# Kernel tuning notes

Measured on AMD Instinct MI355X. Metric: run time of the kernel, lower is better.

Reference implementation:

```python
import jax, jax.numpy as jnp
import numpy as np

N, E = 50000, 500000
DH, DL = 13, 128          # handcrafted / learned node feature dims
OH, OL = 32, 96           # node-encoder output dims; node_dim D = OH+OL
D = OH + OL               # 128
EIN = (DH + DL) + 1 + 3 * D + 1  # 527, forced by concat in forward
H = 256                   # MLP hidden width
HC = 64                   # classifier hidden width
EPS = 1e-8


def _mlp(x, W1, b1, W2, b2):
    # 2-layer MLP with ReLU, matching repo MLP(fc_dims=[H, out])
    return jax.nn.relu(x @ W1 + b1) @ W2 + b2


def _cosine(a, b):
    # torch.nn.CosineSimilarity(dim=1, eps=1e-8)
    na = jnp.maximum(jnp.linalg.norm(a, axis=-1), EPS)
    nb = jnp.maximum(jnp.linalg.norm(b, axis=-1), EPS)
    return jnp.sum(a * b, axis=-1) / (na * nb)


def _lin(key, fan_in, fan_out):
    kW, kb = jax.random.split(key)
    s = 1.0 / np.sqrt(fan_in)
    return (jax.random.uniform(kW, (fan_in, fan_out), jnp.float32, -s, s),
            jax.random.uniform(kb, (fan_out,), jnp.float32, -s, s))


def setup_inputs() -> dict:
    key = jax.random.key(0)
    ks = jax.random.split(key, 16)
    x1 = jax.random.normal(ks[0], (N, DH), jnp.float32)
    x2 = jax.random.normal(ks[1], (N, DL), jnp.float32)
    edge_index = jax.random.randint(ks[2], (2, E), 0, N, jnp.int64)
    Wh1, bh1 = _lin(ks[3], DH, H);   Wh2, bh2 = _lin(ks[4], H, OH)
    Wl1, bl1 = _lin(ks[5], DL, H);   Wl2, bl2 = _lin(ks[6], H, OL)
    We1, be1 = _lin(ks[7], EIN, H);  We2, be2 = _lin(ks[8], H, D)
    Wmsg, bmsg = _lin(ks[9], 2 * D, D)
    Wnode, bnode = _lin(ks[10], 2 * D, D)
    Wmp1, bmp1 = _lin(ks[11], 3 * D, H); Wmp2, bmp2 = _lin(ks[12], H, D)
    Wc1, bc1 = _lin(ks[13], D, HC);  Wc2, bc2 = _lin(ks[14], HC, 1)
    return dict(x1=x1, x2=x2, edge_index=edge_index,
                Wh1=Wh1, bh1=bh1, Wh2=Wh2, bh2=bh2,
                Wl1=Wl1, bl1=bl1, Wl2=Wl2, bl2=bl2,
                We1=We1, be1=be1, We2=We2, be2=be2,
                Wmsg=Wmsg, bmsg=bmsg, Wnode=Wnode, bnode=bnode,
                Wmp1=Wmp1, bmp1=bmp1, Wmp2=Wmp2, bmp2=bmp2,
                Wc1=Wc1, bc1=bc1, Wc2=Wc2, bc2=bc2)


def reference(x1, x2, edge_index,
              Wh1, bh1, Wh2, bh2,
              Wl1, bl1, Wl2, bl2,
              We1, be1, We2, be2,
              Wmsg, bmsg, Wnode, bnode,
              Wmp1, bmp1, Wmp2, bmp2,
              Wc1, bc1, Wc2, bc2):
    src, trg = edge_index[0], edge_index[1]
    # raw-feature edge descriptors
    x_init = jnp.concatenate((x1, x2), axis=-1)            # [N, 141]
    xi_s, xi_t = x_init[src], x_init[trg]                  # gathers [E, 141]
    sim1 = _cosine(xi_s, xi_t)                             # [E]
    abs_init = jnp.abs(xi_s - xi_t)                        # [E, 141]
    # node encoders
    h1 = _mlp(x1, Wh1, bh1, Wh2, bh2)                      # [N, 32]
    h2 = _mlp(x2, Wl1, bl1, Wl2, bl2)                      # [N, 96]
    x = jnp.concatenate((h1, h2), axis=-1)                 # [N, 128]
    xs, xt = x[src], x[trg]                                # [E, 128]
    sim2 = _cosine(xs, xt)                                 # [E]
    edge_feat_in = jnp.concatenate(
        (abs_init, sim1[:, None], xs, xt, jnp.abs(xs - xt), sim2[:, None]),
        axis=-1)                                           # [E, 527]
    e = _mlp(edge_feat_in, We1, be1, We2, be2)             # [E, 128]
    # edge MPNN round: edge->node aggregation, node update, edge update
    msg = jax.nn.relu(jnp.concatenate((xs, e), axis=-1) @ Wmsg + bmsg)  # [E, 128]
    agg = jax.ops.segment_sum(msg, trg, num_segments=N)    # [N, 128]
    xn = jax.nn.relu(jnp.concatenate((x, agg), axis=-1) @ Wnode + bnode)  # [N, 128]
    e_mp = _mlp(jnp.concatenate((xn[src], xn[trg], e), axis=-1),
                Wmp1, bmp1, Wmp2, bmp2)                    # [E, 128]
    pred = _mlp(e_mp, Wc1, bc1, Wc2, bc2)                  # [E, 1]
    return jnp.squeeze(pred, axis=-1)                      # [E]
```

## Files before the change

kernel.cpp:

```cpp
#include <hip/hip_runtime.h>
#include <hip/hip_bf16.h>
#include <hip/hip_fp16.h>


using fp16 = __half;
typedef _Float16 h16;
typedef _Float16 f16x8 __attribute__((ext_vector_type(8)));
typedef _Float16 h16x2 __attribute__((ext_vector_type(2)));
typedef short s16x8 __attribute__((ext_vector_type(8)));
typedef float f32x4 __attribute__((ext_vector_type(4)));

#define NN 50000
#define EE 500000
#define EPSC 1e-8f
#define SCAN_B 196

__device__ __forceinline__ float reluf(float v){ return v > 0.f ? v : 0.f; }

__device__ __forceinline__ float dot8(const f16x8 a, const f16x8 b, float acc)
{
#pragma unroll
  for (int i = 0; i < 4; ++i) {
    const h16x2 av = {a[2 * i], a[2 * i + 1]};
    const h16x2 bv = {b[2 * i], b[2 * i + 1]};
    acc = __builtin_amdgcn_fdot2(av, bv, acc, false);
  }
  return acc;
}

__device__ __forceinline__ f16x8 absdiff8(const f16x8 a, const f16x8 b)
{
  const f16x8 d = a - b;
  s16x8 di = __builtin_bit_cast(s16x8, d);
  di &= (short)0x7fff;
  return __builtin_bit_cast(f16x8, di);
}

#define OFF_E1   0
#define OFF_E2   139264
#define OFF_MSG  172032
#define OFF_NODE 204800
#define OFF_MP1  237568
#define OFF_MP2  335872
#define OFF_C1   368640
#define OFF_N1   376832
#define OFF_N2   458752
#define N2_END   491520
#define WT_TOTAL 524288
#define BF_TOTAL 640

__global__ __launch_bounds__(256) void k_prep(
    const float* __restrict__ We1, const float* __restrict__ We2,
    const float* __restrict__ Wmsg, const float* __restrict__ Wnode,
    const float* __restrict__ Wmp1, const float* __restrict__ Wmp2,
    const float* __restrict__ Wc1,
    const float* __restrict__ Wh1, const float* __restrict__ Wl1,
    const float* __restrict__ Wh2, const float* __restrict__ Wl2,
    const float* __restrict__ bh1, const float* __restrict__ bl1,
    const float* __restrict__ bh2, const float* __restrict__ bl2,
    h16* __restrict__ WT, float* __restrict__ BF)
{
  int idx = blockIdx.x * 256 + threadIdx.x;
  if (idx >= WT_TOTAL) {
    const int b = idx - WT_TOTAL;
    if (b < 512) BF[b] = (b < 256) ? bh1[b] : bl1[b - 256];
    else if (b < BF_TOTAL) {
      const int c = b - 512;
      BF[b] = (c < 32) ? bh2[c] : bl2[c - 32];
    }
    return;
  }
  h16 v;
  if (idx < OFF_E2) {
    const int L = idx, n = L / 544, k = L % 544;
    int r;
    if      (k < 128) r = 142 + k;
    else if (k < 256) r = 270 + (k - 128);
    else if (k < 384) r = 398 + (k - 256);
    else if (k < 512) r = 13 + (k - 384);
    else if (k < 525) r = k - 512;
    else if (k == 528) r = 141;
    else if (k == 529) r = 526;
    else r = -1;
    v = (h16)((r >= 0) ? We1[r * 256 + n] : 0.f);
  } else if (idx < OFF_MSG) {
    const int L = idx - OFF_E2, n = L >> 8, k = L & 255;
    v = (h16)We2[k * 128 + n];
  } else if (idx < OFF_NODE) {
    const int L = idx - OFF_MSG, n = L >> 8, k = L & 255;
    const int ko = (k < 128) ? (128 + k) : (k - 128);
    v = (h16)Wmsg[ko * 128 + n];
  } else if (idx < OFF_MP1) {
    const int L = idx - OFF_NODE, n = L >> 8, k = L & 255;
    v = (h16)Wnode[k * 128 + n];
  } else if (idx < OFF_MP2) {
    const int L = idx - OFF_MP1, n = L / 384, k = L % 384;
    v = (h16)Wmp1[k * 256 + n];
  } else if (idx < OFF_C1) {
    const int L = idx - OFF_MP2, n = L >> 8, k = L & 255;
    v = (h16)Wmp2[k * 128 + n];
  } else if (idx < OFF_N1) {
    const int L = idx - OFF_C1, n = L >> 7, k = L & 127;
    v = (h16)Wc1[k * 64 + n];
  } else if (idx < OFF_N2) {
    const int L = idx - OFF_N1, n = L / 160, k = L % 160;
    float f = 0.f;
    if (n < 256) { if (k < 13) f = Wh1[k * 256 + n]; }
    else { if (k >= 16 && k < 144) f = Wl1[(k - 16) * 256 + (n - 256)]; }
    v = (h16)f;
  } else if (idx < N2_END) {
    const int L = idx - OFF_N2, n = L >> 8, k = L & 255;
    v = (h16)((n < 32) ? Wh2[k * 32 + n] : Wl2[k * 96 + (n - 32)]);
  } else {
    v = (h16)0.f;
  }
  WT[idx] = v;
}

__global__ __launch_bounds__(256) void k_cvt(
    const float* __restrict__ x1, const float* __restrict__ x2,
    const int* __restrict__ ei,
    h16* __restrict__ X1P, h16* __restrict__ X2H, int* __restrict__ CNT)
{
  const int idx = blockIdx.x * 256 + threadIdx.x;
  if (idx < EE) atomicAdd(&CNT[ei[EE + idx]], 1);
  if (idx < NN * 16) {
    const int nn = idx >> 4, j = idx & 15;
    X1P[idx] = (h16)((j < 13) ? x1[nn * 13 + j] : 0.f);
  }
  const int i2 = idx - NN * 16;
  if (i2 >= 0 && i2 < NN * 128) X2H[i2] = (h16)x2[i2];
}

__global__ __launch_bounds__(256) void k_scanA(
    const int* __restrict__ CNT, int* __restrict__ TEX, int* __restrict__ BS)
{
  __shared__ int sd[256];
  const int tid = threadIdx.x;
  const int i = blockIdx.x * 256 + tid;
  const int v = (i < NN) ? CNT[i] : 0;
  sd[tid] = v;
  __syncthreads();
  for (int off = 1; off < 256; off <<= 1) {
    const int x = (tid >= off) ? sd[tid - off] : 0;
    __syncthreads();
    sd[tid] += x;
    __syncthreads();
  }
  if (i < NN) TEX[i] = sd[tid] - v;
  if (tid == 255) BS[blockIdx.x] = sd[255];
}

__global__ __launch_bounds__(256) void k_scanB(
    const int* __restrict__ BS, int* __restrict__ BSSE)
{
  __shared__ int sd[256];
  const int tid = threadIdx.x;
  const int v = (tid < SCAN_B) ? BS[tid] : 0;
  sd[tid] = v;
  __syncthreads();
  for (int off = 1; off < 256; off <<= 1) {
    const int x = (tid >= off) ? sd[tid - off] : 0;
    __syncthreads();
    sd[tid] += x;
    __syncthreads();
  }
  if (tid < SCAN_B) BSSE[tid] = sd[tid] - v;
}

__global__ __launch_bounds__(256) void k_scatter(
    const int* __restrict__ ei, const int* __restrict__ TEX,
    const int* __restrict__ BSSE, int* __restrict__ POS,
    int* __restrict__ ES, int* __restrict__ ET, int* __restrict__ OID)
{
  const int e = blockIdx.x * 256 + threadIdx.x;
  if (e >= EE) return;
  const int t = ei[EE + e];
  const int p = atomicAdd(&POS[t], 1);
  const int idx = BSSE[t >> 8] + TEX[t] + p;
  ES[idx] = ei[e];
  ET[idx] = t;
  OID[idx] = e;
}

template<int ROWS, int UDIM, int KP, int LDA, int WAVES, int RS, bool RELU,
         bool ENDSYNC, int ACOLS = 0, int AOFF = 0, typename F>
__device__ __forceinline__ void mfma_gemm(const h16* sA,
    const h16* __restrict__ WT, const float* __restrict__ bias, F emit)
{
  constexpr int CS = WAVES / RS;
  constexpr int RG = ROWS / RS;
  constexpr int RT = RG / 16;
  constexpr int NPW0 = UDIM / CS;
  constexpr int NPW = (NPW0 < 16) ? 16 : NPW0;
  constexpr int NT = NPW / 16;
  constexpr int NSTEPS = KP / 32;
  constexpr int CH0 = (NT >= 8) ? 1 : ((NT >= 4) ? 2 : 4);
  constexpr int CHUNK = (NSTEPS < CH0) ? NSTEPS : CH0;
  constexpr int NCH = (NSTEPS + CHUNK - 1) / CHUNK;
  const int tid = threadIdx.x;
  const int wave = tid >> 6;
  const int lane = tid & 63;
  const int m = lane & 15;
  const int quad = lane >> 4;
  const int wr = wave % RS;
  const int wc = wave / RS;
  const int rbase = wr * RG;
  const int n0 = wc * NPW;
  const bool active = (n0 < UDIM);
  const int aoff = (ACOLS > 0 && n0 >= ACOLS) ? AOFF : 0;

  f32x4 acc[RT][NT];
#pragma unroll
  for (int r = 0; r < RT; ++r)
#pragma unroll
    for (int j = 0; j < NT; ++j) acc[r][j] = (f32x4){0.f, 0.f, 0.f, 0.f};
  float bb[NT];

  if (active) {
    const h16* wbase = &WT[(size_t)(n0 + m) * KP + quad * 8];
#pragma unroll
    for (int j = 0; j < NT; ++j) bb[j] = bias[n0 + j * 16 + m];

    f16x8 breg[2][CHUNK][NT];
#pragma unroll
    for (int s = 0; s < CHUNK; ++s)
      if (s < NSTEPS)
#pragma unroll
        for (int j = 0; j < NT; ++j)
          breg[0][s][j] = *(const f16x8*)&wbase[(size_t)j * 16 * KP + s * 32];
    asm volatile("" ::: "memory");

#pragma unroll
    for (int c = 0; c < NCH; ++c) {
      if (c + 1 < NCH) {
#pragma unroll
        for (int s = 0; s < CHUNK; ++s) {
          const int st = (c + 1) * CHUNK + s;
          if (st < NSTEPS)
#pragma unroll
            for (int j = 0; j < NT; ++j)
              breg[(c + 1) & 1][s][j] =
                  *(const f16x8*)&wbase[(size_t)j * 16 * KP + st * 32];
        }
      }
#pragma unroll
      for (int s = 0; s < CHUNK; ++s) {
        const int st = c * CHUNK + s;
        if (st < NSTEPS) {
          const int k0 = st * 32;
#pragma unroll
          for (int r = 0; r < RT; ++r) {
            const f16x8 af = *(const f16x8*)&sA[(rbase + r * 16 + m) * LDA + aoff + k0 + quad * 8];
#pragma unroll
            for (int j = 0; j < NT; ++j)
              acc[r][j] = __builtin_amdgcn_mfma_f32_16x16x32_f16(af, breg[c & 1][s][j], acc[r][j], 0, 0, 0);
          }
        }
      }
      asm volatile("" ::: "memory");
    }
  }
  __syncthreads();
  if (active) {
#pragma unroll
    for (int j = 0; j < NT; ++j) {
      const int col = n0 + j * 16 + m;
#pragma unroll
      for (int r = 0; r < RT; ++r)
#pragma unroll
        for (int g = 0; g < 4; ++g) {
          const int row = rbase + r * 16 + quad * 4 + g;
          float v = acc[r][j][g] + bb[j];
          if (RELU) v = reluf(v);
          emit(row, col, v);
        }
    }
  }
  if (ENDSYNC) __syncthreads();
}

__global__ __launch_bounds__(512, 4) void k_nenc(
    const h16* __restrict__ X1P, const h16* __restrict__ X2H,
    const h16* __restrict__ WT, const float* __restrict__ BF,
    h16* __restrict__ XH)
{
  __shared__ __align__(16) h16 sA[32 * 168];
  __shared__ __align__(16) h16 sH[32 * 520];
  const int tid = threadIdx.x;
  const int n0 = blockIdx.x * 32;
  const int remn = NN - n0;
  const int cnt = remn < 32 ? remn : 32;
  const int n = tid >> 4;
  const int q = tid & 15;

  if (n < cnt) {
    const int node = n0 + n;
    if (q < 2)
      *(f16x8*)&sA[n * 168 + q * 8] = *(const f16x8*)&X1P[node * 16 + q * 8];
    else if (q < 4)
      *(f16x8*)&sA[n * 168 + 144 + (q - 2) * 8] = (f16x8){};
    *(f16x8*)&sA[n * 168 + 16 + q * 8] =
        *(const f16x8*)&X2H[(size_t)node * 128 + q * 8];
  }
  __syncthreads();

  mfma_gemm<32, 512, 160, 168, 8, 1, true, true>(sA, WT + OFF_N1, BF,
      [&](int row, int col, float v) { sH[row * 520 + col] = (h16)v; });
  mfma_gemm<32, 128, 256, 520, 8, 1, false, false, 32, 256>(sH, WT + OFF_N2, BF + 512,
      [&](int row, int col, float v) {
        if (row < cnt) XH[(size_t)(n0 + row) * 128 + col] = (h16)v;
      });
}

__global__ __launch_bounds__(512, 4) void k_edge_mlp(
    const h16* __restrict__ X1P, const h16* __restrict__ X2H,
    const int* __restrict__ ES, const int* __restrict__ ET,
    const h16* __restrict__ XH, const h16* __restrict__ WT,
    const float* __restrict__ be1, const float* __restrict__ be2,
    const float* __restrict__ bmsg,
    h16* __restrict__ EB, float* __restrict__ AGG)
{
  __shared__ __align__(16) h16 sFeat[64 * 568];
  __shared__ int strg[64];
  const int tid = threadIdx.x;
  const long e0 = (long)blockIdx.x * 64;
  const long rem = (long)EE - e0;
  const int cnt = rem < 64 ? (int)rem : 64;
  const int n = tid >> 3;
  const int q = tid & 7;
  h16* Arow = &sFeat[n * 568];
  f16x8 xsv0 = {}, xsv1 = {};

  if (n < cnt) {
    const int s = ES[e0 + n];
    const int t = ET[e0 + n];
    if (q == 0) strg[n] = t;
    float ds = 0.f, ns = 0.f, nt = 0.f;
    if (q < 2) {
      const f16x8 a = *(const f16x8*)&X1P[s * 16 + q * 8];
      const f16x8 b = *(const f16x8*)&X1P[t * 16 + q * 8];
      ds = dot8(a, b, ds); ns = dot8(a, a, ns); nt = dot8(b, b, nt);
      *(f16x8*)&Arow[512 + q * 8] = absdiff8(a, b);
    }
#pragma unroll
    for (int c = 0; c < 2; ++c) {
      const f16x8 a = *(const f16x8*)&X2H[(size_t)s * 128 + q * 16 + c * 8];
      const f16x8 b = *(const f16x8*)&X2H[(size_t)t * 128 + q * 16 + c * 8];
      ds = dot8(a, b, ds); ns = dot8(a, a, ns); nt = dot8(b, b, nt);
      *(f16x8*)&Arow[384 + q * 16 + c * 8] = absdiff8(a, b);
    }
    ds += __shfl_xor(ds, 1); ds += __shfl_xor(ds, 2); ds += __shfl_xor(ds, 4);
    ns += __shfl_xor(ns, 1); ns += __shfl_xor(ns, 2); ns += __shfl_xor(ns, 4);
    nt += __shfl_xor(nt, 1); nt += __shfl_xor(nt, 2); nt += __shfl_xor(nt, 4);
    if (q == 0)
      Arow[528] = (h16)(ds / (fmaxf(sqrtf(ns), EPSC) * fmaxf(sqrtf(nt), EPSC)));

    float ds2 = 0.f, ns2 = 0.f, nt2 = 0.f;
#pragma unroll
    for (int c = 0; c < 2; ++c) {
      const f16x8 a = *(const f16x8*)&XH[(size_t)s * 128 + q * 16 + c * 8];
      const f16x8 b = *(const f16x8*)&XH[(size_t)t * 128 + q * 16 + c * 8];
      if (c == 0) xsv0 = a; else xsv1 = a;
      ds2 = dot8(a, b, ds2); ns2 = dot8(a, a, ns2); nt2 = dot8(b, b, nt2);
      *(f16x8*)&Arow[q * 16 + c * 8]       = a;
      *(f16x8*)&Arow[128 + q * 16 + c * 8] = b;
      *(f16x8*)&Arow[256 + q * 16 + c * 8] = absdiff8(a, b);
    }
    ds2 += __shfl_xor(ds2, 1); ds2 += __shfl_xor(ds2, 2); ds2 += __shfl_xor(ds2, 4);
    ns2 += __shfl_xor(ns2, 1); ns2 += __shfl_xor(ns2, 2); ns2 += __shfl_xor(ns2, 4);
    nt2 += __shfl_xor(nt2, 1); nt2 += __shfl_xor(nt2, 2); nt2 += __shfl_xor(nt2, 4);
    if (q == 0)
      Arow[529] = (h16)(ds2 / (fmaxf(sqrtf(ns2), EPSC) * fmaxf(sqrtf(nt2), EPSC)));
    for (int j = 530 + q; j < 544; j += 8) Arow[j] = (h16)0.f;
  } else {
    if (q == 0) strg[n] = 0;
    for (int j8 = q; j8 < 71; j8 += 8) *(f16x8*)&Arow[j8 * 8] = (f16x8){};
  }
  __syncthreads();

  h16* sHid = sFeat;
  mfma_gemm<64, 256, 544, 568, 8, 1, true, true>(sFeat, WT + OFF_E1, be1,
      [&](int row, int col, float v) { sHid[row * 264 + col] = (h16)v; });
  mfma_gemm<64, 128, 256, 264, 8, 1, false, false>(sHid, WT + OFF_E2, be2,
      [&](int row, int col, float v) {
        const h16 vh = (h16)v;
        if (row < cnt) EB[(size_t)(e0 + row) * 128 + col] = vh;
        sHid[row * 264 + col] = vh;
      });
  *(f16x8*)&sFeat[n * 264 + 128 + q * 16]     = xsv0;
  *(f16x8*)&sFeat[n * 264 + 128 + q * 16 + 8] = xsv1;
  __syncthreads();
  mfma_gemm<64, 128, 256, 264, 8, 1, true, true>(sFeat, WT + OFF_MSG, bmsg,
      [&](int row, int col, float v) {
        *(float*)((char*)sFeat + row * 528 + col * 4) = v;
      });
  {
    const int c = tid & 127;
    const int g = tid >> 7;
    const int r0 = g * 16;
    if (r0 < cnt) {
      const int rend = (r0 + 16 < cnt) ? r0 + 16 : cnt;
      float acc = 0.f;
      int cur = strg[r0];
      for (int r = r0; r < rend; ++r) {
        const int t = strg[r];
        if (t != cur) {
          atomicAdd(&AGG[(size_t)cur * 128 + c], acc);
          acc = 0.f; cur = t;
        }
        acc += *(const float*)((const char*)sFeat + r * 528 + c * 4);
      }
      atomicAdd(&AGG[(size_t)cur * 128 + c], acc);
    }
  }
}

__global__ __launch_bounds__(256, 4) void k_node_update(
    const h16* __restrict__ XH, const float* __restrict__ AGG,
    const h16* __restrict__ WT, const float* __restrict__ bnode,
    h16* __restrict__ XNH)
{
  __shared__ __align__(16) h16 sA[64 * 264];
  const int tid = threadIdx.x;
  const int n0 = blockIdx.x * 64;
  const int remn = NN - n0;
  const int cnt = remn < 64 ? remn : 64;
  const int n = tid >> 2;
  const int q = tid & 3;

  if (n < cnt) {
    const f16x8* xr = (const f16x8*)&XH[(size_t)(n0 + n) * 128];
    const float4* ar = (const float4*)&AGG[(size_t)(n0 + n) * 128];
    for (int j8 = q; j8 < 16; j8 += 4)
      *(f16x8*)&sA[n * 264 + j8 * 8] = xr[j8];
    for (int j4 = q; j4 < 32; j4 += 4) {
      const float4 b = ar[j4];
      h16* p1 = &sA[n * 264 + 128 + j4 * 4];
      p1[0] = (h16)b.x; p1[1] = (h16)b.y; p1[2] = (h16)b.z; p1[3] = (h16)b.w;
    }
  } else {
    for (int j = q; j < 256; j += 4) sA[n * 264 + j] = (h16)0.f;
  }
  __syncthreads();

  mfma_gemm<64, 128, 256, 264, 4, 1, true, false>(sA, WT + OFF_NODE, bnode,
      [&](int row, int col, float v) {
        if (row < cnt) XNH[(size_t)(n0 + row) * 128 + col] = (h16)v;
      });
}

__global__ __launch_bounds__(1024, 4) void k_empl(
    const int* __restrict__ ES, const int* __restrict__ ET,
    const int* __restrict__ OID, const h16* __restrict__ XNH,
    const h16* __restrict__ EB, const h16* __restrict__ WT,
    const float* __restrict__ bmp1, const float* __restrict__ bmp2,
    const float* __restrict__ bc1,
    const float* __restrict__ Wc2, const float* __restrict__ bc2,
    float* __restrict__ out)
{
  __shared__ __align__(16) h16 sF[128 * 392];
  const int tid = threadIdx.x;
  const long e0 = (long)blockIdx.x * 128;
  const long rem = (long)EE - e0;
  const int cnt = rem < 128 ? (int)rem : 128;
  const int n = tid >> 3;
  const int q = tid & 7;

  if (n < cnt) {
    const int s = ES[e0 + n];
    const int t = ET[e0 + n];
    const f16x8* xsr = (const f16x8*)&XNH[(size_t)s * 128];
    const f16x8* xtr = (const f16x8*)&XNH[(size_t)t * 128];
    const f16x8* ebr = (const f16x8*)&EB[(size_t)(e0 + n) * 128];
#pragma unroll
    for (int j8 = q; j8 < 16; j8 += 8) {
      *(f16x8*)&sF[n * 392 + j8 * 8]       = xsr[j8];
      *(f16x8*)&sF[n * 392 + 128 + j8 * 8] = xtr[j8];
      *(f16x8*)&sF[n * 392 + 256 + j8 * 8] = ebr[j8];
    }
  } else {
    for (int j8 = q; j8 < 49; j8 += 8) *(f16x8*)&sF[n * 392 + j8 * 8] = (f16x8){};
  }
  __syncthreads();

  h16*  sH2 = sF;
  h16*  sE  = sF;
  float* sHC = (float*)((char*)sF + 34816);
  mfma_gemm<128, 256, 384, 392, 16, 1, true, true>(sF, WT + OFF_MP1, bmp1,
      [&](int row, int col, float v) { sH2[row * 264 + col] = (h16)v; });
  mfma_gemm<128, 128, 256, 264, 16, 1, false, true>(sH2, WT + OFF_MP2, bmp2,
      [&](int row, int col, float v) { sE[row * 136 + col] = (h16)v; });
  mfma_gemm<128, 64, 128, 136, 16, 1, true, true>(sE, WT + OFF_C1, bc1,
      [&](int row, int col, float v) { sHC[row * 65 + col] = v; });
  if (tid < cnt) {
    float acc = bc2[0];
    for (int k = 0; k < 64; ++k) acc += sHC[tid * 65 + k] * Wc2[k];
    out[OID[e0 + tid]] = acc;
  }
}

extern "C" void kernel_launch(void* const* d_in, const int* in_sizes, int n_in,
                              void* d_out, int out_size, void* d_ws, size_t ws_size,
                              hipStream_t stream)
{
  const float* x1  = (const float*)d_in[0];
  const float* x2  = (const float*)d_in[1];
  const int*   ei  = (const int*)d_in[2];
  const float* Wh1 = (const float*)d_in[3],  *bh1 = (const float*)d_in[4];
  const float* Wh2 = (const float*)d_in[5],  *bh2 = (const float*)d_in[6];
  const float* Wl1 = (const float*)d_in[7],  *bl1 = (const float*)d_in[8];
  const float* Wl2 = (const float*)d_in[9],  *bl2 = (const float*)d_in[10];
  const float* We1 = (const float*)d_in[11], *be1 = (const float*)d_in[12];
  const float* We2 = (const float*)d_in[13], *be2 = (const float*)d_in[14];
  const float* Wmsg = (const float*)d_in[15], *bmsg = (const float*)d_in[16];
  const float* Wnode = (const float*)d_in[17], *bnode = (const float*)d_in[18];
  const float* Wmp1 = (const float*)d_in[19], *bmp1 = (const float*)d_in[20];
  const float* Wmp2 = (const float*)d_in[21], *bmp2 = (const float*)d_in[22];
  const float* Wc1 = (const float*)d_in[23], *bc1 = (const float*)d_in[24];
  const float* Wc2 = (const float*)d_in[25], *bc2 = (const float*)d_in[26];
  float* out = (float*)d_out;

  float* AGG = (float*)d_ws;
  h16*   EB  = (h16*)(AGG + (size_t)NN * 128);
  h16*   WT  = EB + (size_t)EE * 128;
  h16*   XH  = WT + WT_TOTAL;
  h16*   XNH = XH + (size_t)NN * 128;
  h16*   X1P = XNH + (size_t)NN * 128;
  h16*   X2H = X1P + (size_t)NN * 16;
  float* BF  = (float*)(X2H + (size_t)NN * 128);
  int*   CNT = (int*)(BF + BF_TOTAL);
  int*   POS = CNT + NN;
  int*   TEX = POS + NN;
  int*   ES  = TEX + NN;
  int*   ET  = ES + EE;
  int*   OID = ET + EE;
  int*   BS  = OID + EE;
  int*   BSSE = BS + 256;

  k_prep<<<(WT_TOTAL + BF_TOTAL + 255) / 256, 256, 0, stream>>>(
      We1, We2, Wmsg, Wnode, Wmp1, Wmp2, Wc1,
      Wh1, Wl1, Wh2, Wl2, bh1, bl1, bh2, bl2, WT, BF);
  hipMemsetAsync(AGG, 0, (size_t)NN * 128 * sizeof(float), stream);
  hipMemsetAsync(CNT, 0, (size_t)2 * NN * sizeof(int), stream);
  k_cvt<<<(NN * 16 + NN * 128 + 255) / 256, 256, 0, stream>>>(
      x1, x2, ei, X1P, X2H, CNT);
  k_scanA<<<SCAN_B, 256, 0, stream>>>(CNT, TEX, BS);
  k_scanB<<<1, 256, 0, stream>>>(BS, BSSE);
  k_scatter<<<(EE + 255) / 256, 256, 0, stream>>>(ei, TEX, BSSE, POS, ES, ET, OID);
  k_nenc<<<(NN + 31) / 32, 512, 0, stream>>>(X1P, X2H, WT, BF, XH);
  k_edge_mlp<<<7813, 512, 0, stream>>>(X1P, X2H, ES, ET, XH, WT,
                                       be1, be2, bmsg, EB, AGG);
  k_node_update<<<782, 256, 0, stream>>>(XH, AGG, WT, bnode, XNH);
  k_empl<<<3907, 1024, 0, stream>>>(ES, ET, OID, XNH, EB, WT, bmp1, bmp2, bc1,
                                    Wc2, bc2, out);
}
```

Before: 842.7 us.

## Split edge-MLP first GEMM into two K-phases to shrink LDS footprint

The first GEMM of k_empl (K=384) is split into two phases: xs/xt first, then the edge embedding is loaded into the same shared-memory columns for the second phase. This cuts the shared tile from 392 to 264 halves per row, so more 1024-thread blocks can be resident per CU, and the launch bound is raised to match. Separately, the two memsets are folded into k_prep and k_cvt, and the block-sum scan kernel is merged into k_scatter to remove launches. The cost is extra barriers inside the split GEMM, a redundant per-block scan in k_scatter, and possible register pressure from the tighter launch bound.

```diff
diff --git a/kernel.cpp b/kernel.cpp
--- a/kernel.cpp
+++ b/kernel.cpp
@@ -41,6 +41,7 @@
 #define OFF_MSG  172032
 #define OFF_NODE 204800
 #define OFF_MP1  237568
+#define OFF_MP1B 303104
 #define OFF_MP2  335872
 #define OFF_C1   368640
 #define OFF_N1   376832
@@ -58,9 +59,10 @@
     const float* __restrict__ Wh2, const float* __restrict__ Wl2,
     const float* __restrict__ bh1, const float* __restrict__ bl1,
     const float* __restrict__ bh2, const float* __restrict__ bl2,
-    h16* __restrict__ WT, float* __restrict__ BF)
+    h16* __restrict__ WT, float* __restrict__ BF, int* __restrict__ CNT)
 {
   int idx = blockIdx.x * 256 + threadIdx.x;
+  if (idx < 2 * NN) CNT[idx] = 0;
   if (idx >= WT_TOTAL) {
     const int b = idx - WT_TOTAL;
     if (b < 512) BF[b] = (b < 256) ? bh1[b] : bl1[b - 256];
@@ -93,9 +95,12 @@
   } else if (idx < OFF_MP1) {
     const int L = idx - OFF_NODE, n = L >> 8, k = L & 255;
     v = (h16)Wnode[k * 128 + n];
+  } else if (idx < OFF_MP1B) {
+    const int L = idx - OFF_MP1, n = L >> 8, k = L & 255;
+    v = (h16)Wmp1[k * 256 + n];
   } else if (idx < OFF_MP2) {
-    const int L = idx - OFF_MP1, n = L / 384, k = L % 384;
-    v = (h16)Wmp1[k * 256 + n];
+    const int L = idx - OFF_MP1B, n = L >> 7, k = L & 127;
+    v = (h16)Wmp1[(256 + k) * 256 + n];
   } else if (idx < OFF_C1) {
     const int L = idx - OFF_MP2, n = L >> 8, k = L & 255;
     v = (h16)Wmp2[k * 128 + n];
@@ -120,10 +125,12 @@
 __global__ __launch_bounds__(256) void k_cvt(
     const float* __restrict__ x1, const float* __restrict__ x2,
     const int* __restrict__ ei,
-    h16* __restrict__ X1P, h16* __restrict__ X2H, int* __restrict__ CNT)
+    h16* __restrict__ X1P, h16* __restrict__ X2H, int* __restrict__ CNT,
+    float* __restrict__ AGG)
 {
   const int idx = blockIdx.x * 256 + threadIdx.x;
   if (idx < EE) atomicAdd(&CNT[ei[EE + idx]], 1);
+  if (idx < NN * 128) AGG[idx] = 0.f;
   if (idx < NN * 16) {
     const int nn = idx >> 4, j = idx & 15;
     X1P[idx] = (h16)((j < 13) ? x1[nn * 13 + j] : 0.f);
@@ -151,36 +158,80 @@
   if (tid == 255) BS[blockIdx.x] = sd[255];
 }
 
-__global__ __launch_bounds__(256) void k_scanB(
-    const int* __restrict__ BS, int* __restrict__ BSSE)
-{
-  __shared__ int sd[256];
-  const int tid = threadIdx.x;
-  const int v = (tid < SCAN_B) ? BS[tid] : 0;
-  sd[tid] = v;
-  __syncthreads();
-  for (int off = 1; off < 256; off <<= 1) {
-    const int x = (tid >= off) ? sd[tid - off] : 0;
-    __syncthreads();
-    sd[tid] += x;
-    __syncthreads();
-  }
-  if (tid < SCAN_B) BSSE[tid] = sd[tid] - v;
-}
-
 __global__ __launch_bounds__(256) void k_scatter(
     const int* __restrict__ ei, const int* __restrict__ TEX,
-    const int* __restrict__ BSSE, int* __restrict__ POS,
+    const int* __restrict__ BS, int* __restrict__ POS,
     int* __restrict__ ES, int* __restrict__ ET, int* __restrict__ OID)
 {
-  const int e = blockIdx.x * 256 + threadIdx.x;
+  __shared__ int sbase[256];
+  const int tid = threadIdx.x;
+  const int v = (tid < SCAN_B) ? BS[tid] : 0;
+  sbase[tid] = v;
+  __syncthreads();
+  for (int off = 1; off < 256; off <<= 1) {
+    const int x = (tid >= off) ? sbase[tid - off] : 0;
+    __syncthreads();
+    sbase[tid] += x;
+    __syncthreads();
+  }
+  const int excl = sbase[tid] - v;
+  __syncthreads();
+  sbase[tid] = excl;
+  __syncthreads();
+
+  const int e = blockIdx.x * 256 + tid;
   if (e >= EE) return;
   const int t = ei[EE + e];
   const int p = atomicAdd(&POS[t], 1);
-  const int idx = BSSE[t >> 8] + TEX[t] + p;
+  const int idx = sbase[t >> 8] + TEX[t] + p;
   ES[idx] = ei[e];
   ET[idx] = t;
   OID[idx] = e;
+}
+
+template<int RT, int NT, int KP, int LDA, int CHUNK>
+__device__ __forceinline__ void gemm_phase(const h16* sA, const h16* wbase,
+    f32x4 (&acc)[RT][NT], int m, int quad)
+{
+  constexpr int NSTEPS = KP / 32;
+  constexpr int NCH = (NSTEPS + CHUNK - 1) / CHUNK;
+  f16x8 breg[2][CHUNK][NT];
+#pragma unroll
+  for (int s = 0; s < CHUNK; ++s)
+    if (s < NSTEPS)
+#pragma unroll
+      for (int j = 0; j < NT; ++j)
+        breg[0][s][j] = *(const f16x8*)&wbase[(size_t)j * 16 * KP + s * 32];
+  asm volatile("" ::: "memory");
+#pragma unroll
+  for (int c = 0; c < NCH; ++c) {
+    if (c + 1 < NCH) {
+#pragma unroll
+      for (int s = 0; s < CHUNK; ++s) {
+        const int st = (c + 1) * CHUNK + s;
+        if (st < NSTEPS)
+#pragma unroll
+          for (int j = 0; j < NT; ++j)
+            breg[(c + 1) & 1][s][j] =
+                *(const f16x8*)&wbase[(size_t)j * 16 * KP + st * 32];
+      }
+    }
+#pragma unroll
+    for (int s = 0; s < CHUNK; ++s) {
+      const int st = c * CHUNK + s;
+      if (st < NSTEPS) {
+        const int k0 = st * 32;
+#pragma unroll
+        for (int r = 0; r < RT; ++r) {
+          const f16x8 af = *(const f16x8*)&sA[(r * 16 + m) * LDA + k0 + quad * 8];
+#pragma unroll
+          for (int j = 0; j < NT; ++j)
+            acc[r][j] = __builtin_amdgcn_mfma_f32_16x16x32_f16(af, breg[c & 1][s][j], acc[r][j], 0, 0, 0);
+        }
+      }
+    }
+    asm volatile("" ::: "memory");
+  }
 }
 
 template<int ROWS, int UDIM, int KP, int LDA, int WAVES, int RS, bool RELU,
@@ -197,7 +248,6 @@
   constexpr int NSTEPS = KP / 32;
   constexpr int CH0 = (NT >= 8) ? 1 : ((NT >= 4) ? 2 : 4);
   constexpr int CHUNK = (NSTEPS < CH0) ? NSTEPS : CH0;
-  constexpr int NCH = (NSTEPS + CHUNK - 1) / CHUNK;
   const int tid = threadIdx.x;
   const int wave = tid >> 6;
   const int lane = tid & 63;
@@ -221,45 +271,7 @@
     const h16* wbase = &WT[(size_t)(n0 + m) * KP + quad * 8];
 #pragma unroll
     for (int j = 0; j < NT; ++j) bb[j] = bias[n0 + j * 16 + m];
-
-    f16x8 breg[2][CHUNK][NT];
-#pragma unroll
-    for (int s = 0; s < CHUNK; ++s)
-      if (s < NSTEPS)
-#pragma unroll
-        for (int j = 0; j < NT; ++j)
-          breg[0][s][j] = *(const f16x8*)&wbase[(size_t)j * 16 * KP + s * 32];
-    asm volatile("" ::: "memory");
-
-#pragma unroll
-    for (int c = 0; c < NCH; ++c) {
-      if (c + 1 < NCH) {
-#pragma unroll
-        for (int s = 0; s < CHUNK; ++s) {
-          const int st = (c + 1) * CHUNK + s;
-          if (st < NSTEPS)
-#pragma unroll
-            for (int j = 0; j < NT; ++j)
-              breg[(c + 1) & 1][s][j] =
-                  *(const f16x8*)&wbase[(size_t)j * 16 * KP + st * 32];
-        }
-      }
-#pragma unroll
-      for (int s = 0; s < CHUNK; ++s) {
-        const int st = c * CHUNK + s;
-        if (st < NSTEPS) {
-          const int k0 = st * 32;
-#pragma unroll
-          for (int r = 0; r < RT; ++r) {
-            const f16x8 af = *(const f16x8*)&sA[(rbase + r * 16 + m) * LDA + aoff + k0 + quad * 8];
-#pragma unroll
-            for (int j = 0; j < NT; ++j)
-              acc[r][j] = __builtin_amdgcn_mfma_f32_16x16x32_f16(af, breg[c & 1][s][j], acc[r][j], 0, 0, 0);
-          }
-        }
-      }
-      asm volatile("" ::: "memory");
-    }
+    gemm_phase<RT, NT, KP, LDA, CHUNK>(&sA[rbase * LDA + aoff], wbase, acc, m, quad);
   }
   __syncthreads();
   if (active) {
@@ -278,6 +290,63 @@
     }
   }
   if (ENDSYNC) __syncthreads();
+}
+
+template<int ROWS, int UDIM, int KP1, int KP2, int LDA, int WAVES, bool RELU,
+         typename S, typename F>
+__device__ __forceinline__ void mfma_gemm_2p(const h16* sA,
+    const h16* __restrict__ WT1, const h16* __restrict__ WT2,
+    const float* __restrict__ bias, S stage2, F emit)
+{
+  constexpr int RT = ROWS / 16;
+  constexpr int NPW0 = UDIM / WAVES;
+  constexpr int NPW = (NPW0 < 16) ? 16 : NPW0;
+  constexpr int NT = NPW / 16;
+  const int tid = threadIdx.x;
+  const int wave = tid >> 6;
+  const int lane = tid & 63;
+  const int m = lane & 15;
+  const int quad = lane >> 4;
+  const int n0 = wave * NPW;
+  const bool active = (n0 < UDIM);
+
+  f32x4 acc[RT][NT];
+#pragma unroll
+  for (int r = 0; r < RT; ++r)
+#pragma unroll
+    for (int j = 0; j < NT; ++j) acc[r][j] = (f32x4){0.f, 0.f, 0.f, 0.f};
+  float bb[NT];
+
+  if (active) {
+#pragma unroll
+    for (int j = 0; j < NT; ++j) bb[j] = bias[n0 + j * 16 + m];
+    gemm_phase<RT, NT, KP1, LDA, 2>(sA,
+        &WT1[(size_t)(n0 + m) * KP1 + quad * 8], acc, m, quad);
+  }
+  __syncthreads();
+  stage2();
+  __syncthreads();
+  if (active) {
+    gemm_phase<RT, NT, KP2, LDA, 2>(sA,
+        &WT2[(size_t)(n0 + m) * KP2 + quad * 8], acc, m, quad);
+  }
+  __syncthreads();
+  if (active) {
+#pragma unroll
+    for (int j = 0; j < NT; ++j) {
+      const int col = n0 + j * 16 + m;
+#pragma unroll
+      for (int r = 0; r < RT; ++r)
+#pragma unroll
+        for (int g = 0; g < 4; ++g) {
+          const int row = r * 16 + quad * 4 + g;
+          float v = acc[r][j][g] + bb[j];
+          if (RELU) v = reluf(v);
+          emit(row, col, v);
+        }
+    }
+  }
+  __syncthreads();
 }
 
 __global__ __launch_bounds__(512, 4) void k_nenc(
@@ -450,7 +519,7 @@
       });
 }
 
-__global__ __launch_bounds__(1024, 4) void k_empl(
+__global__ __launch_bounds__(1024, 8) void k_empl(
     const int* __restrict__ ES, const int* __restrict__ ET,
     const int* __restrict__ OID, const h16* __restrict__ XNH,
     const h16* __restrict__ EB, const h16* __restrict__ WT,
@@ -459,7 +528,7 @@
     const float* __restrict__ Wc2, const float* __restrict__ bc2,
     float* __restrict__ out)
 {
-  __shared__ __align__(16) h16 sF[128 * 392];
+  __shared__ __align__(16) h16 sF[128 * 264];
   const int tid = threadIdx.x;
   const long e0 = (long)blockIdx.x * 128;
   const long rem = (long)EE - e0;
@@ -472,24 +541,34 @@
     const int t = ET[e0 + n];
     const f16x8* xsr = (const f16x8*)&XNH[(size_t)s * 128];
     const f16x8* xtr = (const f16x8*)&XNH[(size_t)t * 128];
-    const f16x8* ebr = (const f16x8*)&EB[(size_t)(e0 + n) * 128];
-#pragma unroll
-    for (int j8 = q; j8 < 16; j8 += 8) {
-      *(f16x8*)&sF[n * 392 + j8 * 8]       = xsr[j8];
-      *(f16x8*)&sF[n * 392 + 128 + j8 * 8] = xtr[j8];
-      *(f16x8*)&sF[n * 392 + 256 + j8 * 8] = ebr[j8];
-    }
+    *(f16x8*)&sF[n * 264 + q * 16]           = xsr[q * 2];
+    *(f16x8*)&sF[n * 264 + q * 16 + 8]       = xsr[q * 2 + 1];
+    *(f16x8*)&sF[n * 264 + 128 + q * 16]     = xtr[q * 2];
+    *(f16x8*)&sF[n * 264 + 128 + q * 16 + 8] = xtr[q * 2 + 1];
   } else {
-    for (int j8 = q; j8 < 49; j8 += 8) *(f16x8*)&sF[n * 392 + j8 * 8] = (f16x8){};
-  }
-  __syncthreads();
-
-  h16*  sH2 = sF;
+    *(f16x8*)&sF[n * 264 + q * 16]           = (f16x8){};
+    *(f16x8*)&sF[n * 264 + q * 16 + 8]       = (f16x8){};
+    *(f16x8*)&sF[n * 264 + 128 + q * 16]     = (f16x8){};
+    *(f16x8*)&sF[n * 264 + 128 + q * 16 + 8] = (f16x8){};
+  }
+  __syncthreads();
+
   h16*  sE  = sF;
-  float* sHC = (float*)((char*)sF + 34816);
-  mfma_gemm<128, 256, 384, 392, 16, 1, true, true>(sF, WT + OFF_MP1, bmp1,
-      [&](int row, int col, float v) { sH2[row * 264 + col] = (h16)v; });
-  mfma_gemm<128, 128, 256, 264, 16, 1, false, true>(sH2, WT + OFF_MP2, bmp2,
+  float* sHC = (float*)sF;
+  mfma_gemm_2p<128, 256, 256, 128, 264, 16, true>(sF,
+      WT + OFF_MP1, WT + OFF_MP1B, bmp1,
+      [&]() {
+        if (n < cnt) {
+          const f16x8* ebr = (const f16x8*)&EB[(size_t)(e0 + n) * 128];
+          *(f16x8*)&sF[n * 264 + q * 16]     = ebr[q * 2];
+          *(f16x8*)&sF[n * 264 + q * 16 + 8] = ebr[q * 2 + 1];
+        } else {
+          *(f16x8*)&sF[n * 264 + q * 16]     = (f16x8){};
+          *(f16x8*)&sF[n * 264 + q * 16 + 8] = (f16x8){};
+        }
+      },
+      [&](int row, int col, float v) { sF[row * 264 + col] = (h16)v; });
+  mfma_gemm<128, 128, 256, 264, 16, 1, false, true>(sF, WT + OFF_MP2, bmp2,
       [&](int row, int col, float v) { sE[row * 136 + col] = (h16)v; });
   mfma_gemm<128, 64, 128, 136, 16, 1, true, true>(sE, WT + OFF_C1, bc1,
       [&](int row, int col, float v) { sHC[row * 65 + col] = v; });
@@ -536,18 +615,14 @@
   int*   ET  = ES + EE;
   int*   OID = ET + EE;
   int*   BS  = OID + EE;
-  int*   BSSE = BS + 256;
 
   k_prep<<<(WT_TOTAL + BF_TOTAL + 255) / 256, 256, 0, stream>>>(
       We1, We2, Wmsg, Wnode, Wmp1, Wmp2, Wc1,
-      Wh1, Wl1, Wh2, Wl2, bh1, bl1, bh2, bl2, WT, BF);
-  hipMemsetAsync(AGG, 0, (size_t)NN * 128 * sizeof(float), stream);
-  hipMemsetAsync(CNT, 0, (size_t)2 * NN * sizeof(int), stream);
+      Wh1, Wl1, Wh2, Wl2, bh1, bl1, bh2, bl2, WT, BF, CNT);
   k_cvt<<<(NN * 16 + NN * 128 + 255) / 256, 256, 0, stream>>>(
-      x1, x2, ei, X1P, X2H, CNT);
+      x1, x2, ei, X1P, X2H, CNT, AGG);
   k_scanA<<<SCAN_B, 256, 0, stream>>>(CNT, TEX, BS);
-  k_scanB<<<1, 256, 0, stream>>>(BS, BSSE);
-  k_scatter<<<(EE + 255) / 256, 256, 0, stream>>>(ei, TEX, BSSE, POS, ES, ET, OID);
+  k_scatter<<<(EE + 255) / 256, 256, 0, stream>>>(ei, TEX, BS, POS, ES, ET, OID);
   k_nenc<<<(NN + 31) / 32, 512, 0, stream>>>(X1P, X2H, WT, BF, XH);
   k_edge_mlp<<<7813, 512, 0, stream>>>(X1P, X2H, ES, ET, XH, WT,
                                        be1, be2, bmsg, EB, AGG);
```

New measurement: 799.3 us. -5.2%, faster.
